# Kernel tuning notes

Hardware: AMD Instinct MI355X
Metric: run time of the kernel (lower is better)

## Reference

```python
import jax, jax.numpy as jnp
import numpy as np

E = 512   # embed_size
H = 512   # hidden_size
V = 32000 # vocab_size
B = 32
P = 196   # num_pixels
T = 32    # seq_len


def setup_inputs() -> dict:
    key = jax.random.key(0)
    ks = jax.random.split(key, 16)
    s = 0.02
    return {
        "features": jax.random.normal(ks[0], (B, P, E), dtype=jnp.float32),
        "captions": jax.random.randint(ks[1], (B, T), 0, V),
        "embed_W": jax.random.normal(ks[2], (V, E), dtype=jnp.float32) * s,
        "attn_W": jax.random.normal(ks[3], (H, E + H), dtype=jnp.float32) * s,
        "attn_b": jnp.zeros((H,), dtype=jnp.float32),
        "v_w": jax.random.normal(ks[4], (H,), dtype=jnp.float32) * s,
        "W_ih": jax.random.normal(ks[5], (4 * H, 2 * E), dtype=jnp.float32) * s,
        "W_hh": jax.random.normal(ks[6], (4 * H, H), dtype=jnp.float32) * s,
        "b_ih": jnp.zeros((4 * H,), dtype=jnp.float32),
        "b_hh": jnp.zeros((4 * H,), dtype=jnp.float32),
        "lin_W": jax.random.normal(ks[7], (V, H), dtype=jnp.float32) * s,
        "lin_b": jnp.zeros((V,), dtype=jnp.float32),
        "inith_W": jax.random.normal(ks[8], (H, E), dtype=jnp.float32) * s,
        "inith_b": jnp.zeros((H,), dtype=jnp.float32),
        "initc_W": jax.random.normal(ks[9], (H, E), dtype=jnp.float32) * s,
        "initc_b": jnp.zeros((H,), dtype=jnp.float32),
    }


def _decode(features, captions, embed_W, attn_W, attn_b, v_w,
            W_ih, W_hh, b_ih, b_hh, lin_W, lin_b,
            inith_W, inith_b, initc_W, initc_b):
    mean_feat = features.mean(axis=1)                       # [B,E]
    h0 = mean_feat @ inith_W.T + inith_b                    # [B,H]
    c0 = mean_feat @ initc_W.T + initc_b                    # [B,H]
    emb = embed_W[captions]                                  # [B,T,E]

    # split attention weight: attn(cat(features, hidden)) = feat@Wf.T + h@Wh.T + b
    Wf = attn_W[:, :E]                                       # [H,E]
    Wh = attn_W[:, E:]                                       # [H,H]
    # features are constant across timesteps: project once
    feat_proj = jnp.einsum('bpe,he->bph', features, Wf)      # [B,P,H]

    def step(carry, x_t):
        h, c = carry
        # Bahdanau attention
        energy = jnp.tanh(feat_proj + (h @ Wh.T)[:, None, :] + attn_b)  # [B,P,H]
        scores = jnp.einsum('bph,h->bp', energy, v_w)                    # [B,P]
        alpha = jax.nn.softmax(scores, axis=1)
        context = jnp.einsum('bp,bpe->be', alpha, features)              # [B,E]
        # LSTM cell (PyTorch gate order i,f,g,o)
        x = jnp.concatenate([x_t, context], axis=-1)                     # [B,2E]
        gates = x @ W_ih.T + b_ih + h @ W_hh.T + b_hh                    # [B,4H]
        i, f, g, o = jnp.split(gates, 4, axis=-1)
        c_new = jax.nn.sigmoid(f) * c + jax.nn.sigmoid(i) * jnp.tanh(g)
        h_new = jax.nn.sigmoid(o) * jnp.tanh(c_new)
        logits = h_new @ lin_W.T + lin_b                                 # [B,V]
        return (h_new, c_new), logits

    xs = jnp.transpose(emb, (1, 0, 2))                        # [T,B,E]
    _, outs = jax.lax.scan(step, (h0, c0), xs)                # [T,B,V]
    return jnp.transpose(outs, (1, 0, 2))                     # [B,T,V]


def reference(features, captions, embed_W, attn_W, attn_b, v_w,
              W_ih, W_hh, b_ih, b_hh, lin_W, lin_b,
              inith_W, inith_b, initc_W, initc_b):
    return _decode(features, captions, embed_W, attn_W, attn_b, v_w,
                   W_ih, W_hh, b_ih, b_hh, lin_W, lin_b,
                   inith_W, inith_b, initc_W, initc_b)
```

## Files before the change

kernel.cpp:

```cpp
#include <hip/hip_runtime.h>

#define E 512
#define H 512
#define V 32000
#define B 32
#define P 196
#define T 32
#define NB 256
#define NT 512

typedef __attribute__((ext_vector_type(8))) short s8v;
typedef __attribute__((ext_vector_type(4))) float f4v;

__device__ __forceinline__ float bf16_to_f(unsigned short u){
  return __uint_as_float(((unsigned)u) << 16);
}
__device__ __forceinline__ unsigned short f_to_bf16(float f){
  unsigned u = __float_as_uint(f);
  u += 0x7FFFu + ((u >> 16) & 1u);
  return (unsigned short)(u >> 16);
}
__device__ __forceinline__ float fast_tanh(float x){
  float e = __expf(2.0f*x);
  return 1.0f - 2.0f/(e + 1.0f);
}
__device__ __forceinline__ float sigmoidf_(float x){
  return 1.0f/(1.0f + __expf(-x));
}
__device__ __forceinline__ void load_lds16(const unsigned short* g, unsigned short* l){
  __builtin_amdgcn_global_load_lds(
      (const __attribute__((address_space(1))) void*)g,
      (__attribute__((address_space(3))) void*)l, 16, 0, 0);
}
__device__ __forceinline__ float dot4(float4 a, float4 b){
  return a.x*b.x + a.y*b.y + a.z*b.z + a.w*b.w;
}

#define AT_SCOPE __HIP_MEMORY_SCOPE_AGENT
__device__ __forceinline__ void cohstore(float* p, float v){
  __hip_atomic_store(p, v, __ATOMIC_RELAXED, AT_SCOPE);
}
__device__ __forceinline__ unsigned cohldu(const unsigned* p){
  return __hip_atomic_load(p, __ATOMIC_RELAXED, AT_SCOPE);
}
__device__ __forceinline__ void cohstu(unsigned* p, unsigned v){
  __hip_atomic_store(p, v, __ATOMIC_RELAXED, AT_SCOPE);
}

__device__ __forceinline__ void bar_arrive(unsigned* my, unsigned gen){
  __syncthreads();
  if (threadIdx.x == 0) cohstu(my, gen);
}
__device__ __forceinline__ void bar_wait(const unsigned* base, unsigned gen){
  if (threadIdx.x < 64){
    for (;;){
      unsigned mn = 0xffffffffu;
      for (int i = (int)threadIdx.x; i < 8; i += 64){
        unsigned v = cohldu(base + i);
        mn = v < mn ? v : mn;
      }
      #pragma unroll
      for (int off = 32; off; off >>= 1){
        unsigned o2 = (unsigned)__shfl_xor((int)mn, off);
        mn = o2 < mn ? o2 : mn;
      }
      if (mn >= gen) break;
      __builtin_amdgcn_s_sleep(2);
    }
    __builtin_amdgcn_sched_barrier(0);
  }
  __syncthreads();
}
__device__ __forceinline__ void bar_mini(unsigned* my, const unsigned* base,
                                         unsigned gen){
  bar_arrive(my, gen);
  bar_wait(base, gen);
}

__global__ void split_kernel(const float* __restrict__ src, int src_ld, int src_coff,
                             int rows,
                             unsigned short* __restrict__ dhi, unsigned short* __restrict__ dlo,
                             int dst_ld, int dst_coff)
{
  int n = rows << 9;
  for (int i = blockIdx.x*blockDim.x + threadIdx.x; i < n; i += gridDim.x*blockDim.x){
    int r = i >> 9, c = i & 511;
    float x = src[(size_t)r*src_ld + src_coff + c];
    unsigned short h = f_to_bf16(x);
    dhi[(size_t)r*dst_ld + dst_coff + c] = h;
    if (dlo) dlo[(size_t)r*dst_ld + dst_coff + c] = f_to_bf16(x - bf16_to_f(h));
  }
}

__global__ void embed_kernel(const int* __restrict__ caps, const float* __restrict__ embW,
                             unsigned short* __restrict__ ehi, unsigned short* __restrict__ elo)
{
  int row = blockIdx.x;
  int cap = caps[row];
  const float* s = embW + (size_t)cap*E;
  for (int e = threadIdx.x; e < E; e += blockDim.x){
    float x = s[e];
    unsigned short h = f_to_bf16(x);
    ehi[(size_t)row*E + e] = h;
    elo[(size_t)row*E + e] = f_to_bf16(x - bf16_to_f(h));
  }
}

__global__ __launch_bounds__(512) void prep_kernel(
    const float* __restrict__ feats,
    const float* __restrict__ inith_W, const float* __restrict__ inith_b,
    const float* __restrict__ initc_W, const float* __restrict__ initc_b,
    float* __restrict__ hgrp, float* __restrict__ c_state)
{
  __shared__ float mf[E];
  const int b = blockIdx.x, tid = threadIdx.x;
  const float* fb = feats + (size_t)b*P*E + tid;
  float s = 0.f;
  for (int p = 0; p < P; ++p) s += fb[(size_t)p*E];
  mf[tid] = s * (1.0f/196.0f);
  __syncthreads();
  const float* wh = inith_W + (size_t)tid*E;
  const float* wc = initc_W + (size_t)tid*E;
  float h0 = inith_b[tid], c0 = initc_b[tid];
  #pragma unroll 4
  for (int e = 0; e < E; e += 4){
    float4 a4 = *(const float4*)(wh + e);
    float4 b4 = *(const float4*)(wc + e);
    float4 m4 = *(const float4*)(mf + e);
    h0 += dot4(a4, m4);
    c0 += dot4(b4, m4);
  }
  hgrp[(size_t)b*512 + tid] = h0;
  c_state[b*512 + tid] = c0;
}

__global__ __launch_bounds__(256) void transpose_wh_kernel(
    const float* __restrict__ attn_W, float* __restrict__ WhT)
{
  __shared__ float tile[64][65];
  const int jt = blockIdx.x & 7, kt = blockIdx.x >> 3;
  const int tx = threadIdx.x & 63, ty = threadIdx.x >> 6;
  for (int r = ty; r < 64; r += 4)
    tile[r][tx] = attn_W[(size_t)(jt*64 + r)*(E+H) + E + kt*64 + tx];
  __syncthreads();
  for (int r = ty; r < 64; r += 4)
    WhT[(size_t)(kt*64 + r)*512 + jt*64 + tx] = tile[tx][r];
}

__global__ __launch_bounds__(256) void pack_wd_kernel(
    const float* __restrict__ Wih, const float* __restrict__ Whh,
    float* __restrict__ Wpack)
{
  __shared__ float tile[64][65];
  const int sub = blockIdx.x & 7, cg = (blockIdx.x >> 3) & 3, kg = blockIdx.x >> 5;
  const int tx = threadIdx.x & 63, ty = threadIdx.x >> 6;
  const int kbase = kg*64;
  for (int cl = ty; cl < 64; cl += 4){
    const int c = cg*64 + cl;
    const int gcol = (c >> 6)*512 + sub*64 + (c & 63);
    const int k = kbase + tx;
    tile[cl][tx] = (k < 512) ? Wih[(size_t)gcol*1024 + 512 + k]
                             : Whh[(size_t)gcol*512 + k - 512];
  }
  __syncthreads();
  for (int kk = ty; kk < 64; kk += 4)
    Wpack[((size_t)sub*1024 + kbase + kk)*256 + cg*64 + tx] = tile[tx][kk];
}

__global__ __launch_bounds__(256) void gemm_bt_kernel(
    const unsigned short* __restrict__ A0, const unsigned short* __restrict__ A1,
    const unsigned short* __restrict__ A2,
    const unsigned short* __restrict__ B0, const unsigned short* __restrict__ B1,
    const unsigned short* __restrict__ B2,
    float* __restrict__ Cc, const float* __restrict__ bias,
    int N, int K, int npasses, int mt, int swz)
{
  __shared__ __align__(16) unsigned short Al[128*32];
  __shared__ __align__(16) unsigned short Bl[128*32];
  const int tid = threadIdx.x;
  const int wid = tid >> 6, l = tid & 63;
  int f = blockIdx.x;
  if (swz) f = (f & 7)*((int)gridDim.x >> 3) + (f >> 3);
  const int m0 = (f % mt)*128, n0 = (f / mt)*128;
  const int wr = wid >> 1, wc = wid & 1;

  f4v acc[4][4];
  #pragma unroll
  for (int i = 0; i < 4; ++i)
    #pragma unroll
    for (int j = 0; j < 4; ++j) acc[i][j] = (f4v){0.f,0.f,0.f,0.f};

  const int s0 = tid, s1 = tid + 256;
  const int r0 = s0 >> 2, g0 = (s0 & 3) ^ ((r0 >> 1) & 3);
  const int r1 = s1 >> 2, g1 = (s1 & 3) ^ ((r1 >> 1) & 3);
  const int la = l & 15, ch = l >> 4;

  for (int pass = 0; pass < npasses; ++pass){
    const unsigned short* Ap = pass == 0 ? A0 : (pass == 1 ? A1 : A2);
    const unsigned short* Bp = pass == 0 ? B0 : (pass == 1 ? B1 : B2);
    for (int k0 = 0; k0 < K; k0 += 32){
      __syncthreads();
      load_lds16(Ap + (size_t)(m0 + r0)*K + k0 + g0*8, Al + s0*8);
      load_lds16(Ap + (size_t)(m0 + r1)*K + k0 + g1*8, Al + s1*8);
      load_lds16(Bp + (size_t)(n0 + r0)*K + k0 + g0*8, Bl + s0*8);
      load_lds16(Bp + (size_t)(n0 + r1)*K + k0 + g1*8, Bl + s1*8);
      __syncthreads();
      s8v av[4], bv[4];
      #pragma unroll
      for (int mi = 0; mi < 4; ++mi){
        int row = wr*64 + mi*16 + la;
        int cs = ch ^ ((row >> 1) & 3);
        av[mi] = *(const s8v*)(Al + (row*4 + cs)*8);
      }
      #pragma unroll
      for (int ni = 0; ni < 4; ++ni){
        int row = wc*64 + ni*16 + la;
        int cs = ch ^ ((row >> 1) & 3);
        bv[ni] = *(const s8v*)(Bl + (row*4 + cs)*8);
      }
      #pragma unroll
      for (int mi = 0; mi < 4; ++mi)
        #pragma unroll
        for (int ni = 0; ni < 4; ++ni)
          acc[mi][ni] = __builtin_amdgcn_mfma_f32_16x16x32_bf16(av[mi], bv[ni], acc[mi][ni], 0, 0, 0);
    }
  }
  #pragma unroll
  for (int mi = 0; mi < 4; ++mi){
    int row = m0 + wr*64 + mi*16 + (l >> 4)*4;
    #pragma unroll
    for (int ni = 0; ni < 4; ++ni){
      int col = n0 + wc*64 + ni*16 + (l & 15);
      float bb = bias ? bias[col] : 0.0f;
      #pragma unroll
      for (int r = 0; r < 4; ++r)
        Cc[(size_t)(row + r)*N + col] = acc[mi][ni][r] + bb;
    }
  }
}

__global__ __launch_bounds__(512, 1) void loop_kernel(
    const float* __restrict__ feats, const float* __restrict__ feat_proj,
    const float* __restrict__ WhT, const float* __restrict__ attn_b,
    const float* __restrict__ v_w, const float* __restrict__ Wpack,
    const float* __restrict__ gates_emb,
    const float* __restrict__ b_ih, const float* __restrict__ b_hh,
    float* __restrict__ hgrp,
    const float* __restrict__ c_init,
    float* __restrict__ ctxbuf,
    float* __restrict__ sps,
    unsigned short* __restrict__ hall_h, unsigned short* __restrict__ hall_l,
    unsigned* __restrict__ fm1, unsigned* __restrict__ fm2, unsigned* __restrict__ fm3)
{
  __shared__ float hs[512];
  __shared__ float ctxl[512];
  __shared__ float hwl[64];
  __shared__ float partA[8][72];
  __shared__ float aux[256];
  __shared__ float biasl[256];
  __shared__ float red[512];
  __shared__ float smx, sinv;

  const int blk = blockIdx.x, tid = threadIdx.x;
  const int b = blk >> 3, sub = blk & 7;
  const int gbase = blk & ~7;
  const int l = tid & 63, wv = tid >> 6;

  float wreg[64];
  #pragma unroll
  for (int kk = 0; kk < 64; ++kk)
    wreg[kk] = WhT[(size_t)(wv*64 + kk)*512 + sub*64 + l];
  float fpreg[25], ftreg[25];
  #pragma unroll
  for (int i = 0; i < 25; ++i){
    const int p = wv + i*8;
    const size_t g = ((size_t)b*P + (p < P ? p : 0))*512 + sub*64 + l;
    fpreg[i] = (p < P) ? feat_proj[g] : 0.f;
    ftreg[i] = (p < P) ? feats[g] : 0.f;
  }
  for (int c = tid; c < 256; c += NT){
    const int gcol = (c >> 6)*512 + sub*64 + (c & 63);
    biasl[c] = b_ih[gcol] + b_hh[gcol];
  }
  const float vl = v_w[sub*64 + l];
  const float ab = (tid < 64) ? attn_b[sub*64 + tid] : 0.f;
  float c_reg = 0.f;
  if (tid < 64) c_reg = c_init[b*512 + sub*64 + tid];

  const int dc = tid & 255;
  const int kh = tid >> 8;
  const float* wp_h = Wpack + ((size_t)sub*1024 + 512 + kh*256)*256 + dc;
  const float* wp_c = Wpack + ((size_t)sub*1024 +       kh*256)*256 + dc;
  __syncthreads();

  for (int t = 0; t < T; ++t){
    const unsigned gen = (unsigned)(t + 1);

    hs[tid] = hgrp[((size_t)t*B + b)*512 + tid];
    __syncthreads();
    {
      const float* hk = hs + wv*64;
      float a = 0.f;
      #pragma unroll
      for (int kk = 0; kk < 64; ++kk) a += hk[kk] * wreg[kk];
      partA[wv][l] = a;
    }
    __syncthreads();
    if (tid < 64){
      float s = ab;
      #pragma unroll
      for (int k = 0; k < 8; ++k) s += partA[k][tid];
      hwl[tid] = s;
    }
    __syncthreads();

    {
      const float hj = hwl[l];
      float* spw = sps + (size_t)(t*B + b)*1600 + sub;
      #pragma unroll
      for (int i = 0; i < 25; ++i){
        const int p = wv + i*8;
        if (p >= P) break;
        float e2 = vl * fast_tanh(fpreg[i] + hj);
        #pragma unroll
        for (int off = 32; off; off >>= 1) e2 += __shfl_xor(e2, off);
        if (l == 0) cohstore(spw + p*8, e2);
      }
    }
    bar_mini(fm1 + blk, fm1 + gbase, gen);

    {
      float sc_v = -1e30f;
      if (tid < P){
        const float* sp = sps + (size_t)(t*B + b)*1600 + tid*8;
        float4 q0 = *(const float4*)sp, q1 = *(const float4*)(sp + 4);
        sc_v = (q0.x + q0.y + q0.z + q0.w) + (q1.x + q1.y + q1.z + q1.w);
      }
      if (tid < 256) aux[tid] = sc_v;
      __syncthreads();
      if (tid < 64){
        float m = -1e30f;
        #pragma unroll
        for (int i = 0; i < 4; ++i) m = fmaxf(m, aux[tid + i*64]);
        #pragma unroll
        for (int off = 32; off; off >>= 1) m = fmaxf(m, __shfl_xor(m, off));
        if (tid == 0) smx = m;
      }
      __syncthreads();
      float al = (tid < P) ? __expf(sc_v - smx) : 0.f;
      if (tid < 256) aux[tid] = al;
      __syncthreads();
      if (tid < 64){
        float s = 0.f;
        #pragma unroll
        for (int i = 0; i < 4; ++i) s += aux[tid + i*64];
        #pragma unroll
        for (int off = 32; off; off >>= 1) s += __shfl_xor(s, off);
        if (tid == 0) sinv = 1.0f/s;
      }
      __syncthreads();
      float a = 0.f;
      #pragma unroll
      for (int i = 0; i < 25; ++i){
        const int p = wv + i*8;
        if (p >= P) break;
        a += aux[p] * ftreg[i];
      }
      partA[wv][l] = a;
      __syncthreads();
      if (tid < 64){
        float s = 0.f;
        #pragma unroll
        for (int k = 0; k < 8; ++k) s += partA[k][tid];
        cohstore(ctxbuf + ((size_t)t*B + b)*512 + sub*64 + tid, s * sinv);
      }
    }
    bar_arrive(fm2 + blk, gen);

    float acc0 = 0.f, acc1 = 0.f, acc2 = 0.f, acc3 = 0.f;
    {
      const float* hk = hs + kh*256;
      #pragma unroll 8
      for (int k = 0; k < 256; k += 4){
        acc0 += wp_h[(size_t)(k+0)*256] * hk[k+0];
        acc1 += wp_h[(size_t)(k+1)*256] * hk[k+1];
        acc2 += wp_h[(size_t)(k+2)*256] * hk[k+2];
        acc3 += wp_h[(size_t)(k+3)*256] * hk[k+3];
      }
    }
    bar_wait(fm2 + gbase, gen);

    ctxl[tid] = ctxbuf[((size_t)t*B + b)*512 + tid];
    __syncthreads();
    {
      const float* ck = ctxl + kh*256;
      #pragma unroll 8
      for (int k = 0; k < 256; k += 4){
        acc0 += wp_c[(size_t)(k+0)*256] * ck[k+0];
        acc1 += wp_c[(size_t)(k+1)*256] * ck[k+1];
        acc2 += wp_c[(size_t)(k+2)*256] * ck[k+2];
        acc3 += wp_c[(size_t)(k+3)*256] * ck[k+3];
      }
      red[dc*2 + kh] = (acc0 + acc1) + (acc2 + acc3);
    }
    __syncthreads();
    if (tid < 64){
      const float* ge = gates_emb + ((size_t)b*T + t)*2048;
      float gv[4];
      #pragma unroll
      for (int g = 0; g < 4; ++g){
        const int c = g*64 + tid;
        gv[g] = red[c*2] + red[c*2 + 1] + biasl[c] + ge[g*512 + sub*64 + tid];
      }
      const float i_ = sigmoidf_(gv[0]);
      const float f_ = sigmoidf_(gv[1]);
      const float g_ = fast_tanh(gv[2]);
      const float o_ = sigmoidf_(gv[3]);
      const int j = sub*64 + tid;
      const float c_new = f_*c_reg + i_*g_;
      const float h_new = o_*fast_tanh(c_new);
      c_reg = c_new;
      cohstore(hgrp + ((size_t)(t+1)*B + b)*512 + j, h_new);
      const unsigned short hh = f_to_bf16(h_new);
      hall_h[((size_t)b*T + t)*512 + j] = hh;
      hall_l[((size_t)b*T + t)*512 + j] = f_to_bf16(h_new - bf16_to_f(hh));
    }
    bar_mini(fm3 + blk, fm3 + gbase, gen);
  }
}

extern "C" void kernel_launch(void* const* d_in, const int* in_sizes, int n_in,
                              void* d_out, int out_size, void* d_ws, size_t ws_size,
                              hipStream_t stream)
{
  (void)in_sizes; (void)n_in; (void)out_size;
  const float* features = (const float*)d_in[0];
  const int*   captions = (const int*)d_in[1];
  const float* embed_W  = (const float*)d_in[2];
  const float* attn_W   = (const float*)d_in[3];
  const float* attn_b   = (const float*)d_in[4];
  const float* v_w      = (const float*)d_in[5];
  const float* W_ih     = (const float*)d_in[6];
  const float* W_hh     = (const float*)d_in[7];
  const float* b_ih     = (const float*)d_in[8];
  const float* b_hh     = (const float*)d_in[9];
  const float* lin_W    = (const float*)d_in[10];
  const float* lin_b    = (const float*)d_in[11];
  const float* inith_W  = (const float*)d_in[12];
  const float* inith_b  = (const float*)d_in[13];
  const float* initc_W  = (const float*)d_in[14];
  const float* initc_b  = (const float*)d_in[15];

  char* o = (char*)d_out;
  unsigned short* feat_bf   = (unsigned short*)o; o += (size_t)(B*P)*E*2;
  unsigned short* Wf_bf     = (unsigned short*)o; o += (size_t)H*E*2;
  float*          feat_proj = (float*)o;          o += (size_t)(B*P)*H*4;
  unsigned short* emb_hi    = (unsigned short*)o; o += (size_t)(B*T)*E*2;
  unsigned short* emb_lo    = (unsigned short*)o; o += (size_t)(B*T)*E*2;
  unsigned short* Wihe_hi   = (unsigned short*)o; o += (size_t)2048*512*2;
  unsigned short* Wihe_lo   = (unsigned short*)o; o += (size_t)2048*512*2;
  float*          gates_emb = (float*)o;          o += (size_t)(B*T)*2048*4;
  float*          Wpack     = (float*)o;          o += (size_t)8*1024*256*4;

  const size_t SZ_LIN  = (size_t)V*H*2;
  const size_t SZ_HALL = (size_t)(B*T)*H*2;
  const size_t SZ_CTX  = (size_t)T*B*512*4;
  const size_t SZ_HG   = (size_t)(T+1)*B*512*4;
  const size_t SZ_SPS  = (size_t)T*B*200*8*4;
  const size_t SZ_ST   = (size_t)B*H*4;
  const size_t SZ_WHT  = (size_t)H*H*4;
  const size_t SZ_FLG  = 4096;
  const size_t need_wo = SZ_LIN + 2*SZ_HALL + SZ_CTX + SZ_HG + SZ_SPS + SZ_ST + SZ_WHT + SZ_FLG;
  const bool three = (ws_size >= need_wo + SZ_LIN);

  char* w = (char*)d_ws;
  unsigned short* lin_hi  = (unsigned short*)w; w += SZ_LIN;
  unsigned short* lin_lo  = (unsigned short*)w; if (three) w += SZ_LIN;
  unsigned short* hall_hi = (unsigned short*)w; w += SZ_HALL;
  unsigned short* hall_lo = (unsigned short*)w; w += SZ_HALL;
  float*          ctxbuf  = (float*)w;          w += SZ_CTX;
  float*          hgrp    = (float*)w;          w += SZ_HG;
  float*          sps     = (float*)w;          w += SZ_SPS;
  float*          c_state = (float*)w;          w += SZ_ST;
  float*          WhT_ws  = (float*)w;          w += SZ_WHT;
  unsigned*       flags   = (unsigned*)w;       w += SZ_FLG;
  unsigned* fm1 = flags;
  unsigned* fm2 = flags + 256;
  unsigned* fm3 = flags + 512;

  split_kernel<<<2048, 256, 0, stream>>>(features, E, 0, B*P, feat_bf, nullptr, E, 0);
  split_kernel<<<256, 256, 0, stream>>>(attn_W, E+H, 0, H, Wf_bf, nullptr, E, 0);
  split_kernel<<<2048, 256, 0, stream>>>(lin_W, 512, 0, V, lin_hi, three ? lin_lo : nullptr, 512, 0);
  split_kernel<<<1024, 256, 0, stream>>>(W_ih, 1024, 0, 2048, Wihe_hi, Wihe_lo, 512, 0);
  embed_kernel<<<B*T, 256, 0, stream>>>(captions, embed_W, emb_hi, emb_lo);
  prep_kernel<<<B, 512, 0, stream>>>(features, inith_W, inith_b, initc_W, initc_b,
                                     hgrp, c_state);
  transpose_wh_kernel<<<64, 256, 0, stream>>>(attn_W, WhT_ws);
  pack_wd_kernel<<<512, 256, 0, stream>>>(W_ih, W_hh, Wpack);
  hipMemsetAsync(flags, 0, SZ_FLG, stream);

  gemm_bt_kernel<<<(B*P/128)*(E/128), 256, 0, stream>>>(
      feat_bf, feat_bf, feat_bf, Wf_bf, Wf_bf, Wf_bf,
      feat_proj, nullptr, E, E, 1, B*P/128, 0);
  gemm_bt_kernel<<<(B*T/128)*(2048/128), 256, 0, stream>>>(
      emb_hi, emb_lo, emb_hi, Wihe_hi, Wihe_hi, Wihe_lo,
      gates_emb, nullptr, 2048, 512, 3, B*T/128, 1);

  loop_kernel<<<NB, NT, 0, stream>>>(
      features, feat_proj, WhT_ws, attn_b, v_w, Wpack, gates_emb, b_ih, b_hh,
      hgrp, c_state, ctxbuf, sps, hall_hi, hall_lo, fm1, fm2, fm3);

  gemm_bt_kernel<<<(V/128)*(B*T/128), 256, 0, stream>>>(
      hall_hi, hall_lo, hall_hi, lin_hi, lin_hi, three ? lin_lo : lin_hi,
      (float*)d_out, lin_b, V, H, three ? 3 : 2, B*T/128, 1);
}
```

Before: 1.247 ms.

## Precompute feature-times-W_ih context projection and drop per-step context barrier

The change reassociates the context path. The features are projected once through the context half of W_ih with a new 3-pass bf16 GEMM (FW), so each step computes gate contributions as alpha·FW rather than building the context vector, exchanging it across blocks, and multiplying by W_ih. This removes one grid-group barrier and the ctxbuf round trip per timestep. It also overlaps the h·W_hh matvec with the first barrier wait, prefetches gates_emb, moves the hall writes between arrive and wait, and shortens the spin sleep. In exchange it adds a large FW buffer (B·P×2048 floats), and each step must now stream 98 rows of it per thread.

```diff
diff --git a/kernel.cpp b/kernel.cpp
--- a/kernel.cpp
+++ b/kernel.cpp
@@ -65,16 +65,11 @@
         mn = o2 < mn ? o2 : mn;
       }
       if (mn >= gen) break;
-      __builtin_amdgcn_s_sleep(2);
+      __builtin_amdgcn_s_sleep(1);
     }
     __builtin_amdgcn_sched_barrier(0);
   }
   __syncthreads();
-}
-__device__ __forceinline__ void bar_mini(unsigned* my, const unsigned* base,
-                                         unsigned gen){
-  bar_arrive(my, gen);
-  bar_wait(base, gen);
 }
 
 __global__ void split_kernel(const float* __restrict__ src, int src_ld, int src_coff,
@@ -147,9 +142,8 @@
     WhT[(size_t)(kt*64 + r)*512 + jt*64 + tx] = tile[tx][r];
 }
 
-__global__ __launch_bounds__(256) void pack_wd_kernel(
-    const float* __restrict__ Wih, const float* __restrict__ Whh,
-    float* __restrict__ Wpack)
+__global__ __launch_bounds__(256) void pack_whh_kernel(
+    const float* __restrict__ Whh, float* __restrict__ Wpackh)
 {
   __shared__ float tile[64][65];
   const int sub = blockIdx.x & 7, cg = (blockIdx.x >> 3) & 3, kg = blockIdx.x >> 5;
@@ -158,13 +152,11 @@
   for (int cl = ty; cl < 64; cl += 4){
     const int c = cg*64 + cl;
     const int gcol = (c >> 6)*512 + sub*64 + (c & 63);
-    const int k = kbase + tx;
-    tile[cl][tx] = (k < 512) ? Wih[(size_t)gcol*1024 + 512 + k]
-                             : Whh[(size_t)gcol*512 + k - 512];
+    tile[cl][tx] = Whh[(size_t)gcol*512 + kbase + tx];
   }
   __syncthreads();
   for (int kk = ty; kk < 64; kk += 4)
-    Wpack[((size_t)sub*1024 + kbase + kk)*256 + cg*64 + tx] = tile[tx][kk];
+    Wpackh[((size_t)sub*512 + kbase + kk)*256 + cg*64 + tx] = tile[tx][kk];
 }
 
 __global__ __launch_bounds__(256) void gemm_bt_kernel(
@@ -240,20 +232,18 @@
 }
 
 __global__ __launch_bounds__(512, 1) void loop_kernel(
-    const float* __restrict__ feats, const float* __restrict__ feat_proj,
+    const float* __restrict__ feat_proj,
     const float* __restrict__ WhT, const float* __restrict__ attn_b,
-    const float* __restrict__ v_w, const float* __restrict__ Wpack,
-    const float* __restrict__ gates_emb,
+    const float* __restrict__ v_w, const float* __restrict__ Wpackh,
+    const float* __restrict__ FW, const float* __restrict__ gates_emb,
     const float* __restrict__ b_ih, const float* __restrict__ b_hh,
     float* __restrict__ hgrp,
     const float* __restrict__ c_init,
-    float* __restrict__ ctxbuf,
     float* __restrict__ sps,
     unsigned short* __restrict__ hall_h, unsigned short* __restrict__ hall_l,
-    unsigned* __restrict__ fm1, unsigned* __restrict__ fm2, unsigned* __restrict__ fm3)
+    unsigned* __restrict__ fm1, unsigned* __restrict__ fm3)
 {
   __shared__ float hs[512];
-  __shared__ float ctxl[512];
   __shared__ float hwl[64];
   __shared__ float partA[8][72];
   __shared__ float aux[256];
@@ -270,13 +260,11 @@
   #pragma unroll
   for (int kk = 0; kk < 64; ++kk)
     wreg[kk] = WhT[(size_t)(wv*64 + kk)*512 + sub*64 + l];
-  float fpreg[25], ftreg[25];
+  float fpreg[25];
   #pragma unroll
   for (int i = 0; i < 25; ++i){
     const int p = wv + i*8;
-    const size_t g = ((size_t)b*P + (p < P ? p : 0))*512 + sub*64 + l;
-    fpreg[i] = (p < P) ? feat_proj[g] : 0.f;
-    ftreg[i] = (p < P) ? feats[g] : 0.f;
+    fpreg[i] = (p < P) ? feat_proj[((size_t)b*P + p)*512 + sub*64 + l] : 0.f;
   }
   for (int c = tid; c < 256; c += NT){
     const int gcol = (c >> 6)*512 + sub*64 + (c & 63);
@@ -289,12 +277,19 @@
 
   const int dc = tid & 255;
   const int kh = tid >> 8;
-  const float* wp_h = Wpack + ((size_t)sub*1024 + 512 + kh*256)*256 + dc;
-  const float* wp_c = Wpack + ((size_t)sub*1024 +       kh*256)*256 + dc;
+  const int gcol_d = (dc >> 6)*512 + sub*64 + (dc & 63);
+  const float* wp_h = Wpackh + ((size_t)sub*512 + kh*256)*256 + dc;
   __syncthreads();
 
   for (int t = 0; t < T; ++t){
     const unsigned gen = (unsigned)(t + 1);
+
+    float gepre[4];
+    if (tid < 64){
+      const float* ge = gates_emb + ((size_t)b*T + t)*2048;
+      #pragma unroll
+      for (int g = 0; g < 4; ++g) gepre[g] = ge[g*512 + sub*64 + tid];
+    }
 
     hs[tid] = hgrp[((size_t)t*B + b)*512 + tid];
     __syncthreads();
@@ -327,7 +322,20 @@
         if (l == 0) cohstore(spw + p*8, e2);
       }
     }
-    bar_mini(fm1 + blk, fm1 + gbase, gen);
+    bar_arrive(fm1 + blk, gen);
+
+    float acch0 = 0.f, acch1 = 0.f, acch2 = 0.f, acch3 = 0.f;
+    {
+      const float* hk = hs + kh*256;
+      #pragma unroll 8
+      for (int k = 0; k < 256; k += 4){
+        acch0 += wp_h[(size_t)(k+0)*256] * hk[k+0];
+        acch1 += wp_h[(size_t)(k+1)*256] * hk[k+1];
+        acch2 += wp_h[(size_t)(k+2)*256] * hk[k+2];
+        acch3 += wp_h[(size_t)(k+3)*256] * hk[k+3];
+      }
+    }
+    bar_wait(fm1 + gbase, gen);
 
     {
       float sc_v = -1e30f;
@@ -359,58 +367,25 @@
         if (tid == 0) sinv = 1.0f/s;
       }
       __syncthreads();
-      float a = 0.f;
-      #pragma unroll
-      for (int i = 0; i < 25; ++i){
-        const int p = wv + i*8;
-        if (p >= P) break;
-        a += aux[p] * ftreg[i];
-      }
-      partA[wv][l] = a;
-      __syncthreads();
-      if (tid < 64){
-        float s = 0.f;
-        #pragma unroll
-        for (int k = 0; k < 8; ++k) s += partA[k][tid];
-        cohstore(ctxbuf + ((size_t)t*B + b)*512 + sub*64 + tid, s * sinv);
-      }
-    }
-    bar_arrive(fm2 + blk, gen);
-
-    float acc0 = 0.f, acc1 = 0.f, acc2 = 0.f, acc3 = 0.f;
+    }
+
+    float accc = 0.f;
     {
-      const float* hk = hs + kh*256;
-      #pragma unroll 8
-      for (int k = 0; k < 256; k += 4){
-        acc0 += wp_h[(size_t)(k+0)*256] * hk[k+0];
-        acc1 += wp_h[(size_t)(k+1)*256] * hk[k+1];
-        acc2 += wp_h[(size_t)(k+2)*256] * hk[k+2];
-        acc3 += wp_h[(size_t)(k+3)*256] * hk[k+3];
-      }
-    }
-    bar_wait(fm2 + gbase, gen);
-
-    ctxl[tid] = ctxbuf[((size_t)t*B + b)*512 + tid];
+      const float* fwb = FW + ((size_t)b*P + kh*98)*2048 + gcol_d;
+      const float* ax = aux + kh*98;
+      #pragma unroll 7
+      for (int i = 0; i < 98; ++i)
+        accc += ax[i] * fwb[(size_t)i*2048];
+    }
+    red[dc*2 + kh] = ((acch0 + acch1) + (acch2 + acch3)) + accc*sinv;
     __syncthreads();
-    {
-      const float* ck = ctxl + kh*256;
-      #pragma unroll 8
-      for (int k = 0; k < 256; k += 4){
-        acc0 += wp_c[(size_t)(k+0)*256] * ck[k+0];
-        acc1 += wp_c[(size_t)(k+1)*256] * ck[k+1];
-        acc2 += wp_c[(size_t)(k+2)*256] * ck[k+2];
-        acc3 += wp_c[(size_t)(k+3)*256] * ck[k+3];
-      }
-      red[dc*2 + kh] = (acc0 + acc1) + (acc2 + acc3);
-    }
-    __syncthreads();
+
     if (tid < 64){
-      const float* ge = gates_emb + ((size_t)b*T + t)*2048;
       float gv[4];
       #pragma unroll
       for (int g = 0; g < 4; ++g){
         const int c = g*64 + tid;
-        gv[g] = red[c*2] + red[c*2 + 1] + biasl[c] + ge[g*512 + sub*64 + tid];
+        gv[g] = red[c*2] + red[c*2 + 1] + biasl[c] + gepre[g];
       }
       const float i_ = sigmoidf_(gv[0]);
       const float f_ = sigmoidf_(gv[1]);
@@ -422,10 +397,17 @@
       c_reg = c_new;
       cohstore(hgrp + ((size_t)(t+1)*B + b)*512 + j, h_new);
       const unsigned short hh = f_to_bf16(h_new);
-      hall_h[((size_t)b*T + t)*512 + j] = hh;
-      hall_l[((size_t)b*T + t)*512 + j] = f_to_bf16(h_new - bf16_to_f(hh));
-    }
-    bar_mini(fm3 + blk, fm3 + gbase, gen);
+      aux[tid] = __uint_as_float(((unsigned)hh << 16) |
+                 (unsigned)f_to_bf16(h_new - bf16_to_f(hh)));
+    }
+    bar_arrive(fm3 + blk, gen);
+    if (tid < 64){
+      const unsigned pk = __float_as_uint(aux[tid]);
+      const int j = sub*64 + tid;
+      hall_h[((size_t)b*T + t)*512 + j] = (unsigned short)(pk >> 16);
+      hall_l[((size_t)b*T + t)*512 + j] = (unsigned short)(pk & 0xffffu);
+    }
+    bar_wait(fm3 + gbase, gen);
   }
 }
 
@@ -452,25 +434,28 @@
   const float* initc_b  = (const float*)d_in[15];
 
   char* o = (char*)d_out;
-  unsigned short* feat_bf   = (unsigned short*)o; o += (size_t)(B*P)*E*2;
+  unsigned short* feat_hi   = (unsigned short*)o; o += (size_t)(B*P)*E*2;
+  unsigned short* feat_lo   = (unsigned short*)o; o += (size_t)(B*P)*E*2;
   unsigned short* Wf_bf     = (unsigned short*)o; o += (size_t)H*E*2;
   float*          feat_proj = (float*)o;          o += (size_t)(B*P)*H*4;
   unsigned short* emb_hi    = (unsigned short*)o; o += (size_t)(B*T)*E*2;
   unsigned short* emb_lo    = (unsigned short*)o; o += (size_t)(B*T)*E*2;
   unsigned short* Wihe_hi   = (unsigned short*)o; o += (size_t)2048*512*2;
   unsigned short* Wihe_lo   = (unsigned short*)o; o += (size_t)2048*512*2;
+  unsigned short* Wihc_hi   = (unsigned short*)o; o += (size_t)2048*512*2;
+  unsigned short* Wihc_lo   = (unsigned short*)o; o += (size_t)2048*512*2;
   float*          gates_emb = (float*)o;          o += (size_t)(B*T)*2048*4;
-  float*          Wpack     = (float*)o;          o += (size_t)8*1024*256*4;
+  float*          Wpackh    = (float*)o;          o += (size_t)8*512*256*4;
+  float*          FW        = (float*)o;          o += (size_t)(B*P)*2048*4;
 
   const size_t SZ_LIN  = (size_t)V*H*2;
   const size_t SZ_HALL = (size_t)(B*T)*H*2;
-  const size_t SZ_CTX  = (size_t)T*B*512*4;
   const size_t SZ_HG   = (size_t)(T+1)*B*512*4;
   const size_t SZ_SPS  = (size_t)T*B*200*8*4;
   const size_t SZ_ST   = (size_t)B*H*4;
   const size_t SZ_WHT  = (size_t)H*H*4;
   const size_t SZ_FLG  = 4096;
-  const size_t need_wo = SZ_LIN + 2*SZ_HALL + SZ_CTX + SZ_HG + SZ_SPS + SZ_ST + SZ_WHT + SZ_FLG;
+  const size_t need_wo = SZ_LIN + 2*SZ_HALL + SZ_HG + SZ_SPS + SZ_ST + SZ_WHT + SZ_FLG;
   const bool three = (ws_size >= need_wo + SZ_LIN);
 
   char* w = (char*)d_ws;
@@ -478,37 +463,39 @@
   unsigned short* lin_lo  = (unsigned short*)w; if (three) w += SZ_LIN;
   unsigned short* hall_hi = (unsigned short*)w; w += SZ_HALL;
   unsigned short* hall_lo = (unsigned short*)w; w += SZ_HALL;
-  float*          ctxbuf  = (float*)w;          w += SZ_CTX;
   float*          hgrp    = (float*)w;          w += SZ_HG;
   float*          sps     = (float*)w;          w += SZ_SPS;
   float*          c_state = (float*)w;          w += SZ_ST;
   float*          WhT_ws  = (float*)w;          w += SZ_WHT;
   unsigned*       flags   = (unsigned*)w;       w += SZ_FLG;
   unsigned* fm1 = flags;
-  unsigned* fm2 = flags + 256;
-  unsigned* fm3 = flags + 512;
-
-  split_kernel<<<2048, 256, 0, stream>>>(features, E, 0, B*P, feat_bf, nullptr, E, 0);
+  unsigned* fm3 = flags + 256;
+
+  split_kernel<<<2048, 256, 0, stream>>>(features, E, 0, B*P, feat_hi, feat_lo, E, 0);
   split_kernel<<<256, 256, 0, stream>>>(attn_W, E+H, 0, H, Wf_bf, nullptr, E, 0);
   split_kernel<<<2048, 256, 0, stream>>>(lin_W, 512, 0, V, lin_hi, three ? lin_lo : nullptr, 512, 0);
   split_kernel<<<1024, 256, 0, stream>>>(W_ih, 1024, 0, 2048, Wihe_hi, Wihe_lo, 512, 0);
+  split_kernel<<<1024, 256, 0, stream>>>(W_ih, 1024, 512, 2048, Wihc_hi, Wihc_lo, 512, 0);
   embed_kernel<<<B*T, 256, 0, stream>>>(captions, embed_W, emb_hi, emb_lo);
   prep_kernel<<<B, 512, 0, stream>>>(features, inith_W, inith_b, initc_W, initc_b,
                                      hgrp, c_state);
   transpose_wh_kernel<<<64, 256, 0, stream>>>(attn_W, WhT_ws);
-  pack_wd_kernel<<<512, 256, 0, stream>>>(W_ih, W_hh, Wpack);
+  pack_whh_kernel<<<256, 256, 0, stream>>>(W_hh, Wpackh);
   hipMemsetAsync(flags, 0, SZ_FLG, stream);
 
   gemm_bt_kernel<<<(B*P/128)*(E/128), 256, 0, stream>>>(
-      feat_bf, feat_bf, feat_bf, Wf_bf, Wf_bf, Wf_bf,
+      feat_hi, feat_hi, feat_hi, Wf_bf, Wf_bf, Wf_bf,
       feat_proj, nullptr, E, E, 1, B*P/128, 0);
   gemm_bt_kernel<<<(B*T/128)*(2048/128), 256, 0, stream>>>(
       emb_hi, emb_lo, emb_hi, Wihe_hi, Wihe_hi, Wihe_lo,
       gates_emb, nullptr, 2048, 512, 3, B*T/128, 1);
+  gemm_bt_kernel<<<(B*P/128)*(2048/128), 256, 0, stream>>>(
+      feat_hi, feat_lo, feat_hi, Wihc_hi, Wihc_hi, Wihc_lo,
+      FW, nullptr, 2048, 512, 3, B*P/128, 1);
 
   loop_kernel<<<NB, NT, 0, stream>>>(
-      features, feat_proj, WhT_ws, attn_b, v_w, Wpack, gates_emb, b_ih, b_hh,
-      hgrp, c_state, ctxbuf, sps, hall_hi, hall_lo, fm1, fm2, fm3);
+      feat_proj, WhT_ws, attn_b, v_w, Wpackh, FW, gates_emb, b_ih, b_hh,
+      hgrp, c_state, sps, hall_hi, hall_lo, fm1, fm3);
 
   gemm_bt_kernel<<<(V/128)*(B*T/128), 256, 0, stream>>>(
       hall_hi, hall_lo, hall_hi, lin_hi, lin_hi, three ? lin_lo : lin_hi,
```

New measurement: 1.061 ms. -15.0%, faster.
